# Optimization experiments

Hardware: AMD Instinct MI355X
Metric: run time of the kernel (lower is better)

## Reference

```python
import jax, jax.numpy as jnp
import numpy as np

N_NODES = 50000
N_EDGES = 800000
N_DEC = 1000000
D_IN, D_HID, D_OUT = 128, 128, 64


def setup_inputs() -> dict:
    key = jax.random.key(0)
    k = jax.random.split(key, 8)
    x = jax.random.normal(k[0], (N_NODES, D_IN), dtype=jnp.float32)
    # GCNConv linear weights (glorot-ish scale); bias added after aggregation (PyG default)
    W_in = jax.random.normal(k[1], (D_IN, D_HID), dtype=jnp.float32) / np.sqrt(D_IN)
    b_in = jnp.zeros((D_HID,), dtype=jnp.float32)
    W_out = jax.random.normal(k[2], (D_HID, D_OUT), dtype=jnp.float32) / np.sqrt(D_HID)
    b_out = jnp.zeros((D_OUT,), dtype=jnp.float32)
    edge_index = jax.random.randint(k[3], (2, N_EDGES), 0, N_NODES, dtype=jnp.int64)
    edge_label_index = jax.random.randint(k[4], (2, N_DEC), 0, N_NODES, dtype=jnp.int64)
    return {"x": x, "W_in": W_in, "b_in": b_in, "W_out": W_out, "b_out": b_out,
            "edge_index": edge_index, "edge_label_index": edge_label_index}


def reference(x, W_in, b_in, W_out, b_out, edge_index, edge_label_index):
    N = x.shape[0]
    # GCN normalization with self-loops (PyG GCNConv defaults)
    loop = jnp.arange(N, dtype=edge_index.dtype)
    src = jnp.concatenate([edge_index[0], loop])
    dst = jnp.concatenate([edge_index[1], loop])
    deg = jax.ops.segment_sum(jnp.ones_like(dst, dtype=x.dtype), dst, num_segments=N)
    dinv = jnp.where(deg > 0, jax.lax.rsqrt(jnp.maximum(deg, 1e-12)), 0.0)
    norm = (dinv[src] * dinv[dst])[:, None]  # [E+N, 1]

    def gcn(h, W, b):
        h = h @ W                                     # linear (no bias inside)
        agg = jax.ops.segment_sum(h[src] * norm, dst, num_segments=N)
        return agg + b                                # bias after aggregation

    z = jax.nn.relu(gcn(x, W_in, b_in))
    z = jax.nn.relu(gcn(z, W_out, b_out))
    # decoder: gather-multiply-sum over edge pairs -> logits [N_DEC]
    logits = jnp.sum(z[edge_label_index[0]] * z[edge_label_index[1]], axis=-1)
    return logits
```

## Files before the change

kernel.cpp:

```cpp
#include <hip/hip_runtime.h>

#define NN 50000
#define NE 800000
#define ND 1000000
#define DH 128
#define DO 64

#define NB 196
#define BCAPP 6400
#define P1B 196
#define WTB1 25
#define GB1 ((NN + 63) / 64)

typedef _Float16 h16;
typedef h16 h16x4 __attribute__((ext_vector_type(4)));
typedef h16 h16x8 __attribute__((ext_vector_type(8)));
typedef float f32x4 __attribute__((ext_vector_type(4)));
typedef unsigned short u16;

__global__ __launch_bounds__(1024) void k_bucket_wt(
    const int* __restrict__ esrc, const int* __restrict__ edst,
    int* __restrict__ bpk, int* __restrict__ cnt,
    const float* __restrict__ Wi, const float* __restrict__ Wo,
    h16* __restrict__ WiT, h16* __restrict__ WoT,
    h16* __restrict__ h1, h16* __restrict__ h2) {
    if (blockIdx.x < P1B) {
        __shared__ int lcur[NB];
        int t = threadIdx.x;
        if (t < NB) lcur[t] = 0;
        __syncthreads();
        int base = blockIdx.x * 4096;
#pragma unroll
        for (int i = 0; i < 4; ++i) {
            int idx = base + t + i * 1024;
            if (idx < NE) {
                int s = esrc[idx];
                int d = edst[idx];
                int bb = d >> 8;
                int r = atomicAdd(&lcur[bb], 1);
                bpk[((size_t)bb * P1B + blockIdx.x) * 64 + r] =
                    s | ((d & 255) << 16);
            }
        }
        __syncthreads();
        if (t < NB) cnt[blockIdx.x * NB + t] = lcur[t];
    } else {
        int t = (blockIdx.x - P1B) * 1024 + threadIdx.x;
        if (t < 128 * 128) {
            int k = t >> 7, n = t & 127;
            WiT[n * 128 + k] = (h16)Wi[t];
        } else if (t < 128 * 128 + 64 * 128) {
            int t2 = t - 128 * 128;
            int k = t2 >> 6, n = t2 & 63;
            WoT[n * 128 + k] = (h16)Wo[t2];
        } else if (t < 128 * 128 + 64 * 128 + 192) {
            int t3 = t - (128 * 128 + 64 * 128);
            if (t3 < 128) h1[(size_t)NN * DH + t3] = (h16)0.f;
            else          h2[(size_t)NN * DO + (t3 - 128)] = (h16)0.f;
        }
    }
}

template <int BN, bool AF32>
__device__ __forceinline__ void gemm_body(
    const void* __restrict__ Ain, const h16* __restrict__ WT,
    h16* __restrict__ out, int bx, char* sX, char* sW) {
    const int tid = threadIdx.x;
    const int row0 = bx * 64;

#pragma unroll
    for (int i = 0; i < 4; ++i) {
        int c = tid + i * 256;
        int row = c >> 4, kb = c & 15;
        int gr = row0 + row;
        h16x8 v = {};
        if (gr < NN) {
            if (AF32) {
                const float* src = (const float*)Ain + (size_t)gr * 128 + kb * 8;
                float4 u0 = *(const float4*)src;
                float4 u1 = *(const float4*)(src + 4);
                v[0] = (h16)u0.x; v[1] = (h16)u0.y; v[2] = (h16)u0.z; v[3] = (h16)u0.w;
                v[4] = (h16)u1.x; v[5] = (h16)u1.y; v[6] = (h16)u1.z; v[7] = (h16)u1.w;
            } else {
                v = *(const h16x8*)((const h16*)Ain + (size_t)gr * 128 + kb * 8);
            }
        }
        *(h16x8*)(sX + row * 256 + ((kb * 16) ^ ((row & 7) << 4))) = v;
    }
#pragma unroll
    for (int i = 0; i < BN / 16; ++i) {
        int c = tid + i * 256;
        int n = c >> 4, kb = c & 15;
        h16x8 v = *(const h16x8*)&WT[(size_t)n * 128 + kb * 8];
        *(h16x8*)(sW + n * 256 + ((kb * 16) ^ ((n & 7) << 4))) = v;
    }
    __syncthreads();

    const int lane = tid & 63, wv = tid >> 6;
    const int g = lane >> 4, l15 = lane & 15;
    const int r = wv * 16 + l15;
    f32x4 acc[BN / 16];
#pragma unroll
    for (int ct = 0; ct < BN / 16; ++ct) acc[ct] = (f32x4){0.f, 0.f, 0.f, 0.f};

#pragma unroll
    for (int t = 0; t < 4; ++t) {
        int kb2 = t * 64 + g * 16;
        h16x8 a = *(const h16x8*)(sX + r * 256 + (kb2 ^ ((r & 7) << 4)));
#pragma unroll
        for (int ct = 0; ct < BN / 16; ++ct) {
            int n = ct * 16 + l15;
            h16x8 b = *(const h16x8*)(sW + n * 256 + (kb2 ^ ((n & 7) << 4)));
            acc[ct] = __builtin_amdgcn_mfma_f32_16x16x32_f16(a, b, acc[ct], 0, 0, 0);
        }
    }

#pragma unroll
    for (int j = 0; j < 4; ++j) {
        int row = row0 + wv * 16 + g * 4 + j;
        if (row < NN) {
#pragma unroll
            for (int ct = 0; ct < BN / 16; ++ct)
                out[(size_t)row * BN + ct * 16 + l15] = (h16)acc[ct][j];
        }
    }
}

__global__ __launch_bounds__(256) void k_sort_gemm1(
    const int* __restrict__ bpk, const int* __restrict__ cnt,
    int* __restrict__ off, int* __restrict__ degn,
    float* __restrict__ dinv, u16* __restrict__ csrc,
    const float* __restrict__ x, const h16* __restrict__ WiT,
    h16* __restrict__ h1) {
    __shared__ __align__(16) char smem[49152];
    if (blockIdx.x >= NB) {
        gemm_body<DH, true>(x, WiT, h1, blockIdx.x - NB, smem, smem + 16384);
        return;
    }
    int* hist   = (int*)smem;
    int* lofs   = hist + 256;
    int* exc    = lofs + 256;
    int* lcur   = exc + 256;
    int* cbs    = lcur + 256;
    int* scsr32 = cbs + 256;
    u16* scsr16 = (u16*)(scsr32 + 5120);
    int b = blockIdx.x, t = threadIdx.x;
    hist[t] = 0; lcur[t] = 0;
    int cc = (t < P1B) ? cnt[t * NB + b] : 0;
    cbs[t] = cc;
    __syncthreads();
#pragma unroll
    for (int d = 1; d < 256; d <<= 1) {
        int add = (t >= d) ? cbs[t - d] : 0;
        __syncthreads();
        cbs[t] += add;
        __syncthreads();
    }
    int cbase = cbs[t] - cc;
    int craw = cbs[255];
    if (t < P1B) {
        const int* src = bpk + ((size_t)b * P1B + t) * 64;
        for (int i = 0; i < cc; ++i) scsr32[cbase + i] = src[i];
    }
    __syncthreads();
    for (int j = t; j < craw; j += 256)
        atomicAdd(&hist[(scsr32[j] >> 16) & 255], 1);
    __syncthreads();
    int pd = (hist[t] + 7) & ~7;
    lofs[t] = pd;
    __syncthreads();
#pragma unroll
    for (int d = 1; d < 256; d <<= 1) {
        int add = (t >= d) ? lofs[t - d] : 0;
        __syncthreads();
        lofs[t] += add;
        __syncthreads();
    }
    exc[t] = lofs[t] - pd;
    __syncthreads();
    int cntp = lofs[255];
    for (int j = t; j < cntp; j += 256) scsr16[j] = (u16)NN;
    __syncthreads();
    int node = b * 256 + t;
    if (node < NN) {
        off[node] = b * BCAPP + exc[t];
        degn[node] = pd;
        dinv[node] = rsqrtf((float)hist[t] + 1.0f);
    }
    if (b == 0 && t == 0) dinv[NN] = 0.f;
    for (int j = t; j < craw; j += 256) {
        int p = scsr32[j];
        int d = (p >> 16) & 255;
        int r = atomicAdd(&lcur[d], 1);
        scsr16[exc[d] + r] = (u16)(p & 0xFFFF);
    }
    __syncthreads();
    u16* cdst = csrc + (size_t)b * BCAPP;
    for (int j = t; j < cntp / 2; j += 256)
        *(unsigned*)(cdst + 2 * j) = *(const unsigned*)(scsr16 + 2 * j);
}

__global__ __launch_bounds__(256) void k_gemm2(
    const h16* __restrict__ z1, const h16* __restrict__ WoT,
    h16* __restrict__ h2) {
    __shared__ __align__(16) char smem[32768];
    gemm_body<DO, false>(z1, WoT, h2, blockIdx.x, smem, smem + 16384);
}

__global__ __launch_bounds__(256) void k_agg128(
    const h16x4* __restrict__ hs, const float* __restrict__ dinv,
    const int* __restrict__ off, const int* __restrict__ degn,
    const u16* __restrict__ csrc,
    const float* __restrict__ bias, h16x4* __restrict__ z) {
    int node = blockIdx.x * 8 + (threadIdx.x >> 5);
    if (node >= NN) return;
    int col = threadIdx.x & 31;
    int s = off[node], e = s + degn[node];
    float a0 = 0.f, a1 = 0.f, a2 = 0.f, a3 = 0.f;
    for (int j = s; j < e; j += 8) {
        int i0 = csrc[j],     i1 = csrc[j + 1], i2 = csrc[j + 2], i3 = csrc[j + 3];
        int i4 = csrc[j + 4], i5 = csrc[j + 5], i6 = csrc[j + 6], i7 = csrc[j + 7];
        float w0 = dinv[i0], w1 = dinv[i1], w2 = dinv[i2], w3 = dinv[i3];
        float w4 = dinv[i4], w5 = dinv[i5], w6 = dinv[i6], w7 = dinv[i7];
        h16x4 v0 = hs[(size_t)i0 * 32 + col];
        h16x4 v1 = hs[(size_t)i1 * 32 + col];
        h16x4 v2 = hs[(size_t)i2 * 32 + col];
        h16x4 v3 = hs[(size_t)i3 * 32 + col];
        h16x4 v4 = hs[(size_t)i4 * 32 + col];
        h16x4 v5 = hs[(size_t)i5 * 32 + col];
        h16x4 v6 = hs[(size_t)i6 * 32 + col];
        h16x4 v7 = hs[(size_t)i7 * 32 + col];
        a0 = fmaf(w0, (float)v0.x, a0); a1 = fmaf(w0, (float)v0.y, a1);
        a2 = fmaf(w0, (float)v0.z, a2); a3 = fmaf(w0, (float)v0.w, a3);
        a0 = fmaf(w1, (float)v1.x, a0); a1 = fmaf(w1, (float)v1.y, a1);
        a2 = fmaf(w1, (float)v1.z, a2); a3 = fmaf(w1, (float)v1.w, a3);
        a0 = fmaf(w2, (float)v2.x, a0); a1 = fmaf(w2, (float)v2.y, a1);
        a2 = fmaf(w2, (float)v2.z, a2); a3 = fmaf(w2, (float)v2.w, a3);
        a0 = fmaf(w3, (float)v3.x, a0); a1 = fmaf(w3, (float)v3.y, a1);
        a2 = fmaf(w3, (float)v3.z, a2); a3 = fmaf(w3, (float)v3.w, a3);
        a0 = fmaf(w4, (float)v4.x, a0); a1 = fmaf(w4, (float)v4.y, a1);
        a2 = fmaf(w4, (float)v4.z, a2); a3 = fmaf(w4, (float)v4.w, a3);
        a0 = fmaf(w5, (float)v5.x, a0); a1 = fmaf(w5, (float)v5.y, a1);
        a2 = fmaf(w5, (float)v5.z, a2); a3 = fmaf(w5, (float)v5.w, a3);
        a0 = fmaf(w6, (float)v6.x, a0); a1 = fmaf(w6, (float)v6.y, a1);
        a2 = fmaf(w6, (float)v6.z, a2); a3 = fmaf(w6, (float)v6.w, a3);
        a0 = fmaf(w7, (float)v7.x, a0); a1 = fmaf(w7, (float)v7.y, a1);
        a2 = fmaf(w7, (float)v7.z, a2); a3 = fmaf(w7, (float)v7.w, a3);
    }
    float dv = dinv[node];
    h16x4 vs = hs[(size_t)node * 32 + col];
    a0 = fmaf(dv, (float)vs.x, a0); a1 = fmaf(dv, (float)vs.y, a1);
    a2 = fmaf(dv, (float)vs.z, a2); a3 = fmaf(dv, (float)vs.w, a3);
    float4 bb = ((const float4*)bias)[col];
    float r0 = dv * a0 + bb.x, r1 = dv * a1 + bb.y;
    float r2 = dv * a2 + bb.z, r3 = dv * a3 + bb.w;
    h16x4 o;
    o.x = (h16)(r0 > 0.f ? r0 : 0.f); o.y = (h16)(r1 > 0.f ? r1 : 0.f);
    o.z = (h16)(r2 > 0.f ? r2 : 0.f); o.w = (h16)(r3 > 0.f ? r3 : 0.f);
    z[(size_t)node * 32 + col] = o;
}

__global__ __launch_bounds__(256) void k_agg64(
    const h16x4* __restrict__ hs, const float* __restrict__ dinv,
    const int* __restrict__ off, const int* __restrict__ degn,
    const u16* __restrict__ csrc,
    const float* __restrict__ bias, h16x4* __restrict__ z) {
    int node = blockIdx.x * 16 + (threadIdx.x >> 4);
    if (node >= NN) return;
    int col = threadIdx.x & 15;
    int s = off[node], e = s + degn[node];
    float a0 = 0.f, a1 = 0.f, a2 = 0.f, a3 = 0.f;
    for (int j = s; j < e; j += 8) {
        int i0 = csrc[j],     i1 = csrc[j + 1], i2 = csrc[j + 2], i3 = csrc[j + 3];
        int i4 = csrc[j + 4], i5 = csrc[j + 5], i6 = csrc[j + 6], i7 = csrc[j + 7];
        float w0 = dinv[i0], w1 = dinv[i1], w2 = dinv[i2], w3 = dinv[i3];
        float w4 = dinv[i4], w5 = dinv[i5], w6 = dinv[i6], w7 = dinv[i7];
        h16x4 v0 = hs[(size_t)i0 * 16 + col];
        h16x4 v1 = hs[(size_t)i1 * 16 + col];
        h16x4 v2 = hs[(size_t)i2 * 16 + col];
        h16x4 v3 = hs[(size_t)i3 * 16 + col];
        h16x4 v4 = hs[(size_t)i4 * 16 + col];
        h16x4 v5 = hs[(size_t)i5 * 16 + col];
        h16x4 v6 = hs[(size_t)i6 * 16 + col];
        h16x4 v7 = hs[(size_t)i7 * 16 + col];
        a0 = fmaf(w0, (float)v0.x, a0); a1 = fmaf(w0, (float)v0.y, a1);
        a2 = fmaf(w0, (float)v0.z, a2); a3 = fmaf(w0, (float)v0.w, a3);
        a0 = fmaf(w1, (float)v1.x, a0); a1 = fmaf(w1, (float)v1.y, a1);
        a2 = fmaf(w1, (float)v1.z, a2); a3 = fmaf(w1, (float)v1.w, a3);
        a0 = fmaf(w2, (float)v2.x, a0); a1 = fmaf(w2, (float)v2.y, a1);
        a2 = fmaf(w2, (float)v2.z, a2); a3 = fmaf(w2, (float)v2.w, a3);
        a0 = fmaf(w3, (float)v3.x, a0); a1 = fmaf(w3, (float)v3.y, a1);
        a2 = fmaf(w3, (float)v3.z, a2); a3 = fmaf(w3, (float)v3.w, a3);
        a0 = fmaf(w4, (float)v4.x, a0); a1 = fmaf(w4, (float)v4.y, a1);
        a2 = fmaf(w4, (float)v4.z, a2); a3 = fmaf(w4, (float)v4.w, a3);
        a0 = fmaf(w5, (float)v5.x, a0); a1 = fmaf(w5, (float)v5.y, a1);
        a2 = fmaf(w5, (float)v5.z, a2); a3 = fmaf(w5, (float)v5.w, a3);
        a0 = fmaf(w6, (float)v6.x, a0); a1 = fmaf(w6, (float)v6.y, a1);
        a2 = fmaf(w6, (float)v6.z, a2); a3 = fmaf(w6, (float)v6.w, a3);
        a0 = fmaf(w7, (float)v7.x, a0); a1 = fmaf(w7, (float)v7.y, a1);
        a2 = fmaf(w7, (float)v7.z, a2); a3 = fmaf(w7, (float)v7.w, a3);
    }
    float dv = dinv[node];
    h16x4 vs = hs[(size_t)node * 16 + col];
    a0 = fmaf(dv, (float)vs.x, a0); a1 = fmaf(dv, (float)vs.y, a1);
    a2 = fmaf(dv, (float)vs.z, a2); a3 = fmaf(dv, (float)vs.w, a3);
    float4 bb = ((const float4*)bias)[col];
    float r0 = dv * a0 + bb.x, r1 = dv * a1 + bb.y;
    float r2 = dv * a2 + bb.z, r3 = dv * a3 + bb.w;
    h16x4 o;
    o.x = (h16)(r0 > 0.f ? r0 : 0.f); o.y = (h16)(r1 > 0.f ? r1 : 0.f);
    o.z = (h16)(r2 > 0.f ? r2 : 0.f); o.w = (h16)(r3 > 0.f ? r3 : 0.f);
    z[(size_t)node * 16 + col] = o;
}

__global__ __launch_bounds__(256) void k_dec(const h16* __restrict__ z2,
                                             const int* __restrict__ eli,
                                             float* __restrict__ out) {
    int g = blockIdx.x * 32 + (threadIdx.x >> 3);
    int p0 = g * 8;
    if (p0 >= ND) return;
    int sub = threadIdx.x & 7;
    int4 ea0 = *(const int4*)&eli[p0];
    int4 ea1 = *(const int4*)&eli[p0 + 4];
    int4 eb0 = *(const int4*)&eli[ND + p0];
    int4 eb1 = *(const int4*)&eli[ND + p0 + 4];
    int ia[8] = {ea0.x, ea0.y, ea0.z, ea0.w, ea1.x, ea1.y, ea1.z, ea1.w};
    int ib[8] = {eb0.x, eb0.y, eb0.z, eb0.w, eb1.x, eb1.y, eb1.z, eb1.w};
    float v[8];
#pragma unroll
    for (int q = 0; q < 8; ++q) {
        h16x8 va = *(const h16x8*)&z2[(size_t)ia[q] * DO + sub * 8];
        h16x8 vb = *(const h16x8*)&z2[(size_t)ib[q] * DO + sub * 8];
        float acc = 0.f;
#pragma unroll
        for (int k = 0; k < 8; ++k) acc += (float)va[k] * (float)vb[k];
        v[q] = acc;
    }
#pragma unroll
    for (int o = 1; o < 8; o <<= 1) {
#pragma unroll
        for (int q = 0; q < 8; ++q) v[q] += __shfl_xor(v[q], o);
    }
    if (sub == 0) {
        *(float4*)&out[p0] = make_float4(v[0], v[1], v[2], v[3]);
        *(float4*)&out[p0 + 4] = make_float4(v[4], v[5], v[6], v[7]);
    }
}

extern "C" void kernel_launch(void* const* d_in, const int* in_sizes, int n_in,
                              void* d_out, int out_size, void* d_ws, size_t ws_size,
                              hipStream_t stream) {
    const float* x  = (const float*)d_in[0];
    const float* Wi = (const float*)d_in[1];
    const float* bi = (const float*)d_in[2];
    const float* Wo = (const float*)d_in[3];
    const float* bo = (const float*)d_in[4];
    const int* ei   = (const int*)d_in[5];
    const int* eli  = (const int*)d_in[6];
    float* out = (float*)d_out;

    char* ws = (char*)d_ws;
    size_t o = 0;
    auto alloc = [&](size_t bytes) -> char* {
        char* p = ws + o;
        o = (o + bytes + 255) & ~(size_t)255;
        return p;
    };
    float* dinv = (float*)alloc((NN + 1) * 4);
    int* off    = (int*)alloc(NN * 4);
    int* degn   = (int*)alloc(NN * 4);
    int* cnt    = (int*)alloc((size_t)P1B * NB * 4);
    int* bpk    = (int*)alloc((size_t)NB * P1B * 64 * 4);
    u16* csrc   = (u16*)alloc((size_t)NB * BCAPP * 2);
    h16* WiT    = (h16*)alloc(128 * 128 * 2);
    h16* WoT    = (h16*)alloc(64 * 128 * 2);
    h16* h1     = (h16*)alloc((size_t)(NN + 1) * DH * 2);
    h16* z1     = (h16*)alloc((size_t)NN * DH * 2);
    h16* h2     = (h16*)alloc((size_t)(NN + 1) * DO * 2);
    h16* z2     = (h16*)alloc((size_t)NN * DO * 2);

    const int* esrc = ei;
    const int* edst = ei + NE;

    k_bucket_wt<<<P1B + WTB1, 1024, 0, stream>>>(esrc, edst, bpk, cnt, Wi, Wo,
                                                 WiT, WoT, h1, h2);
    k_sort_gemm1<<<NB + GB1, 256, 0, stream>>>(bpk, cnt, off, degn,
                                               dinv, csrc, x, WiT, h1);
    k_agg128<<<(NN + 7) / 8, 256, 0, stream>>>((const h16x4*)h1, dinv, off, degn, csrc, bi, (h16x4*)z1);
    k_gemm2<<<GB1, 256, 0, stream>>>(z1, WoT, h2);
    k_agg64<<<(NN + 15) / 16, 256, 0, stream>>>((const h16x4*)h2, dinv, off, degn, csrc, bo, (h16x4*)z2);

    k_dec<<<(ND / 8 + 31) / 32, 256, 0, stream>>>(z2, eli, out);
}
```

Measured before the change: 95.99 us.

## Fuse layer-1 aggregation with layer-2 GEMM through shared-memory tile

Merges the 128-wide aggregation kernel and the second GEMM into one kernel. Each 512-thread block aggregates 64 nodes into a swizzled LDS tile, then runs MFMA against WoT staged in LDS and writes h2 directly. This removes the z1 round-trip through global memory and one kernel launch. In exchange each warp handles four nodes in sequence, so there is less parallelism and latency hiding in the gather phase, and fewer blocks are launched.

```diff
diff --git a/kernel.cpp b/kernel.cpp
--- a/kernel.cpp
+++ b/kernel.cpp
@@ -200,64 +200,107 @@
         *(unsigned*)(cdst + 2 * j) = *(const unsigned*)(scsr16 + 2 * j);
 }
 
-__global__ __launch_bounds__(256) void k_gemm2(
-    const h16* __restrict__ z1, const h16* __restrict__ WoT,
-    h16* __restrict__ h2) {
-    __shared__ __align__(16) char smem[32768];
-    gemm_body<DO, false>(z1, WoT, h2, blockIdx.x, smem, smem + 16384);
-}
-
-__global__ __launch_bounds__(256) void k_agg128(
+__global__ __launch_bounds__(512) void k_agg_gemm(
     const h16x4* __restrict__ hs, const float* __restrict__ dinv,
     const int* __restrict__ off, const int* __restrict__ degn,
-    const u16* __restrict__ csrc,
-    const float* __restrict__ bias, h16x4* __restrict__ z) {
-    int node = blockIdx.x * 8 + (threadIdx.x >> 5);
-    if (node >= NN) return;
-    int col = threadIdx.x & 31;
-    int s = off[node], e = s + degn[node];
-    float a0 = 0.f, a1 = 0.f, a2 = 0.f, a3 = 0.f;
-    for (int j = s; j < e; j += 8) {
-        int i0 = csrc[j],     i1 = csrc[j + 1], i2 = csrc[j + 2], i3 = csrc[j + 3];
-        int i4 = csrc[j + 4], i5 = csrc[j + 5], i6 = csrc[j + 6], i7 = csrc[j + 7];
-        float w0 = dinv[i0], w1 = dinv[i1], w2 = dinv[i2], w3 = dinv[i3];
-        float w4 = dinv[i4], w5 = dinv[i5], w6 = dinv[i6], w7 = dinv[i7];
-        h16x4 v0 = hs[(size_t)i0 * 32 + col];
-        h16x4 v1 = hs[(size_t)i1 * 32 + col];
-        h16x4 v2 = hs[(size_t)i2 * 32 + col];
-        h16x4 v3 = hs[(size_t)i3 * 32 + col];
-        h16x4 v4 = hs[(size_t)i4 * 32 + col];
-        h16x4 v5 = hs[(size_t)i5 * 32 + col];
-        h16x4 v6 = hs[(size_t)i6 * 32 + col];
-        h16x4 v7 = hs[(size_t)i7 * 32 + col];
-        a0 = fmaf(w0, (float)v0.x, a0); a1 = fmaf(w0, (float)v0.y, a1);
-        a2 = fmaf(w0, (float)v0.z, a2); a3 = fmaf(w0, (float)v0.w, a3);
-        a0 = fmaf(w1, (float)v1.x, a0); a1 = fmaf(w1, (float)v1.y, a1);
-        a2 = fmaf(w1, (float)v1.z, a2); a3 = fmaf(w1, (float)v1.w, a3);
-        a0 = fmaf(w2, (float)v2.x, a0); a1 = fmaf(w2, (float)v2.y, a1);
-        a2 = fmaf(w2, (float)v2.z, a2); a3 = fmaf(w2, (float)v2.w, a3);
-        a0 = fmaf(w3, (float)v3.x, a0); a1 = fmaf(w3, (float)v3.y, a1);
-        a2 = fmaf(w3, (float)v3.z, a2); a3 = fmaf(w3, (float)v3.w, a3);
-        a0 = fmaf(w4, (float)v4.x, a0); a1 = fmaf(w4, (float)v4.y, a1);
-        a2 = fmaf(w4, (float)v4.z, a2); a3 = fmaf(w4, (float)v4.w, a3);
-        a0 = fmaf(w5, (float)v5.x, a0); a1 = fmaf(w5, (float)v5.y, a1);
-        a2 = fmaf(w5, (float)v5.z, a2); a3 = fmaf(w5, (float)v5.w, a3);
-        a0 = fmaf(w6, (float)v6.x, a0); a1 = fmaf(w6, (float)v6.y, a1);
-        a2 = fmaf(w6, (float)v6.z, a2); a3 = fmaf(w6, (float)v6.w, a3);
-        a0 = fmaf(w7, (float)v7.x, a0); a1 = fmaf(w7, (float)v7.y, a1);
-        a2 = fmaf(w7, (float)v7.z, a2); a3 = fmaf(w7, (float)v7.w, a3);
-    }
-    float dv = dinv[node];
-    h16x4 vs = hs[(size_t)node * 32 + col];
-    a0 = fmaf(dv, (float)vs.x, a0); a1 = fmaf(dv, (float)vs.y, a1);
-    a2 = fmaf(dv, (float)vs.z, a2); a3 = fmaf(dv, (float)vs.w, a3);
+    const u16* __restrict__ csrc, const float* __restrict__ bias,
+    const h16* __restrict__ WoT, h16* __restrict__ h2) {
+    __shared__ __align__(16) char smem[32768];
+    char* tile = smem;
+    char* sW = smem + 16384;
+    const int tid = threadIdx.x;
+    const int node0 = blockIdx.x * 64;
+
+#pragma unroll
+    for (int i = 0; i < 2; ++i) {
+        int c = tid + i * 512;
+        int n = c >> 4, kb = c & 15;
+        h16x8 v = *(const h16x8*)&WoT[(size_t)n * 128 + kb * 8];
+        *(h16x8*)(sW + n * 256 + ((kb * 16) ^ ((n & 7) << 4))) = v;
+    }
+
+    int g = tid >> 5, col = tid & 31;
     float4 bb = ((const float4*)bias)[col];
-    float r0 = dv * a0 + bb.x, r1 = dv * a1 + bb.y;
-    float r2 = dv * a2 + bb.z, r3 = dv * a3 + bb.w;
-    h16x4 o;
-    o.x = (h16)(r0 > 0.f ? r0 : 0.f); o.y = (h16)(r1 > 0.f ? r1 : 0.f);
-    o.z = (h16)(r2 > 0.f ? r2 : 0.f); o.w = (h16)(r3 > 0.f ? r3 : 0.f);
-    z[(size_t)node * 32 + col] = o;
+#pragma unroll
+    for (int i = 0; i < 4; ++i) {
+        int lr = g * 4 + i;
+        int node = node0 + lr;
+        h16x4 o = {};
+        if (node < NN) {
+            int s = off[node], e = s + degn[node];
+            float a0 = 0.f, a1 = 0.f, a2 = 0.f, a3 = 0.f;
+            for (int j = s; j < e; j += 8) {
+                int i0 = csrc[j],     i1 = csrc[j + 1], i2 = csrc[j + 2], i3 = csrc[j + 3];
+                int i4 = csrc[j + 4], i5 = csrc[j + 5], i6 = csrc[j + 6], i7 = csrc[j + 7];
+                float w0 = dinv[i0], w1 = dinv[i1], w2 = dinv[i2], w3 = dinv[i3];
+                float w4 = dinv[i4], w5 = dinv[i5], w6 = dinv[i6], w7 = dinv[i7];
+                h16x4 v0 = hs[(size_t)i0 * 32 + col];
+                h16x4 v1 = hs[(size_t)i1 * 32 + col];
+                h16x4 v2 = hs[(size_t)i2 * 32 + col];
+                h16x4 v3 = hs[(size_t)i3 * 32 + col];
+                h16x4 v4 = hs[(size_t)i4 * 32 + col];
+                h16x4 v5 = hs[(size_t)i5 * 32 + col];
+                h16x4 v6 = hs[(size_t)i6 * 32 + col];
+                h16x4 v7 = hs[(size_t)i7 * 32 + col];
+                a0 = fmaf(w0, (float)v0.x, a0); a1 = fmaf(w0, (float)v0.y, a1);
+                a2 = fmaf(w0, (float)v0.z, a2); a3 = fmaf(w0, (float)v0.w, a3);
+                a0 = fmaf(w1, (float)v1.x, a0); a1 = fmaf(w1, (float)v1.y, a1);
+                a2 = fmaf(w1, (float)v1.z, a2); a3 = fmaf(w1, (float)v1.w, a3);
+                a0 = fmaf(w2, (float)v2.x, a0); a1 = fmaf(w2, (float)v2.y, a1);
+                a2 = fmaf(w2, (float)v2.z, a2); a3 = fmaf(w2, (float)v2.w, a3);
+                a0 = fmaf(w3, (float)v3.x, a0); a1 = fmaf(w3, (float)v3.y, a1);
+                a2 = fmaf(w3, (float)v3.z, a2); a3 = fmaf(w3, (float)v3.w, a3);
+                a0 = fmaf(w4, (float)v4.x, a0); a1 = fmaf(w4, (float)v4.y, a1);
+                a2 = fmaf(w4, (float)v4.z, a2); a3 = fmaf(w4, (float)v4.w, a3);
+                a0 = fmaf(w5, (float)v5.x, a0); a1 = fmaf(w5, (float)v5.y, a1);
+                a2 = fmaf(w5, (float)v5.z, a2); a3 = fmaf(w5, (float)v5.w, a3);
+                a0 = fmaf(w6, (float)v6.x, a0); a1 = fmaf(w6, (float)v6.y, a1);
+                a2 = fmaf(w6, (float)v6.z, a2); a3 = fmaf(w6, (float)v6.w, a3);
+                a0 = fmaf(w7, (float)v7.x, a0); a1 = fmaf(w7, (float)v7.y, a1);
+                a2 = fmaf(w7, (float)v7.z, a2); a3 = fmaf(w7, (float)v7.w, a3);
+            }
+            float dv = dinv[node];
+            h16x4 vs = hs[(size_t)node * 32 + col];
+            a0 = fmaf(dv, (float)vs.x, a0); a1 = fmaf(dv, (float)vs.y, a1);
+            a2 = fmaf(dv, (float)vs.z, a2); a3 = fmaf(dv, (float)vs.w, a3);
+            float r0 = dv * a0 + bb.x, r1 = dv * a1 + bb.y;
+            float r2 = dv * a2 + bb.z, r3 = dv * a3 + bb.w;
+            o.x = (h16)(r0 > 0.f ? r0 : 0.f); o.y = (h16)(r1 > 0.f ? r1 : 0.f);
+            o.z = (h16)(r2 > 0.f ? r2 : 0.f); o.w = (h16)(r3 > 0.f ? r3 : 0.f);
+        }
+        *(h16x4*)(tile + lr * 256 + (((col >> 1) * 16) ^ ((lr & 7) << 4)) +
+                  (col & 1) * 8) = o;
+    }
+    __syncthreads();
+
+    int w = tid >> 6, lane = tid & 63;
+    int g4 = lane >> 4, l15 = lane & 15;
+    int rb = (w >> 1) * 16;
+    int ch = (w & 1) * 32;
+    f32x4 acc[2];
+    acc[0] = (f32x4){0.f, 0.f, 0.f, 0.f};
+    acc[1] = (f32x4){0.f, 0.f, 0.f, 0.f};
+#pragma unroll
+    for (int t = 0; t < 4; ++t) {
+        int kb2 = t * 64 + g4 * 16;
+        int r = rb + l15;
+        h16x8 a = *(const h16x8*)(tile + r * 256 + (kb2 ^ ((r & 7) << 4)));
+#pragma unroll
+        for (int ct = 0; ct < 2; ++ct) {
+            int n = ch + ct * 16 + l15;
+            h16x8 bfr = *(const h16x8*)(sW + n * 256 + (kb2 ^ ((n & 7) << 4)));
+            acc[ct] = __builtin_amdgcn_mfma_f32_16x16x32_f16(a, bfr, acc[ct], 0, 0, 0);
+        }
+    }
+#pragma unroll
+    for (int j = 0; j < 4; ++j) {
+        int row = node0 + rb + g4 * 4 + j;
+        if (row < NN) {
+#pragma unroll
+            for (int ct = 0; ct < 2; ++ct)
+                h2[(size_t)row * DO + ch + ct * 16 + l15] = (h16)acc[ct][j];
+        }
+    }
 }
 
 __global__ __launch_bounds__(256) void k_agg64(
@@ -375,7 +418,6 @@
     h16* WiT    = (h16*)alloc(128 * 128 * 2);
     h16* WoT    = (h16*)alloc(64 * 128 * 2);
     h16* h1     = (h16*)alloc((size_t)(NN + 1) * DH * 2);
-    h16* z1     = (h16*)alloc((size_t)NN * DH * 2);
     h16* h2     = (h16*)alloc((size_t)(NN + 1) * DO * 2);
     h16* z2     = (h16*)alloc((size_t)NN * DO * 2);
 
@@ -386,8 +428,8 @@
                                                  WiT, WoT, h1, h2);
     k_sort_gemm1<<<NB + GB1, 256, 0, stream>>>(bpk, cnt, off, degn,
                                                dinv, csrc, x, WiT, h1);
-    k_agg128<<<(NN + 7) / 8, 256, 0, stream>>>((const h16x4*)h1, dinv, off, degn, csrc, bi, (h16x4*)z1);
-    k_gemm2<<<GB1, 256, 0, stream>>>(z1, WoT, h2);
+    k_agg_gemm<<<GB1, 512, 0, stream>>>((const h16x4*)h1, dinv, off, degn,
+                                        csrc, bi, WoT, h2);
     k_agg64<<<(NN + 15) / 16, 256, 0, stream>>>((const h16x4*)h2, dinv, off, degn, csrc, bo, (h16x4*)z2);
 
     k_dec<<<(ND / 8 + 31) / 32, 256, 0, stream>>>(z2, eli, out);
```

Measured after the change: 102.3 us. 6.5% more time.
